# Performance work log

Measured on AMD Instinct MI355X. Metric: run time of the kernel, lower is better.

The kernel has to match this reference:

```python
import jax, jax.numpy as jnp
import numpy as np

B, H = 1_000_000, 18
TEMPERATURE = 1.0
EPS = 1e-8
NEG = -1e9  # stand-in for -inf that keeps logaddexp/exp finite


def setup_inputs() -> dict:
    key = jax.random.key(0)
    k1, k2, k3 = jax.random.split(key, 3)
    scores = jax.random.normal(k1, (B, H), dtype=jnp.float32)
    rankings = jax.random.randint(k2, (B, H), 0, 18, dtype=jnp.int32)
    mask = jax.random.randint(k3, (B, H), 0, 2, dtype=jnp.int32).astype(bool)
    return {"scores": scores, "rankings": rankings, "mask": mask}


def reference(scores, rankings, mask):
    # valid horses: masked-in and ranking >= 0
    valid = mask & (rankings >= 0)                      # (B, H) bool
    num_horses = scores.shape[1]

    # Stable sort valid horses to the front, ordered by ranking (Plackett-Luce order).
    sort_key = jnp.where(valid, rankings, num_horses + 1)
    order = jnp.argsort(sort_key, axis=1)               # stable
    s = jnp.take_along_axis(jnp.clip(scores, -10.0, 10.0), order, axis=1) / TEMPERATURE
    v = jnp.take_along_axis(valid, order, axis=1)
    s = jnp.where(v, s, NEG)                            # invalid horses contribute exp(-1e9)=0

    # Reverse cumulative logsumexp replaces the O(n^2) sequential softmax peel:
    # lse[i] = logsumexp(s[i:])  ->  log P(pick i-th) = s[i] - lse[i]
    lse = jax.lax.associative_scan(jnp.logaddexp, s, reverse=True, axis=1)
    prob = jnp.clip(jnp.exp(s - lse), EPS, 1.0 - EPS)   # matches original per-step prob clamp

    n = jnp.sum(valid, axis=1)                          # (B,) valid horse count
    # positions 0 .. n-2 contribute (last pick is deterministic)
    pos_ok = jnp.arange(num_horses)[None, :] < (n - 1)[:, None]
    race_loss = jnp.sum(jnp.where(pos_ok, -jnp.log(prob), 0.0), axis=1)

    race_valid = n >= 2                                 # races with <2 valid horses skipped
    num = jnp.sum(jnp.where(race_valid, race_loss, 0.0))
    den = jnp.sum(race_valid)
    return jnp.where(den > 0, num / jnp.maximum(den, 1).astype(num.dtype), jnp.float32(0.0))
```

## Files before the change

kernel.cpp:

```cpp
#include <hip/hip_runtime.h>
#include <stdint.h>

#define H 18
#define TPB 256
#define RPB 256

__device__ __forceinline__ void ce(unsigned long long& x, unsigned long long& y) {
    unsigned long long a = x, b = y;
    bool lt = a < b;
    x = lt ? a : b;
    y = lt ? b : a;
}

__global__ __launch_bounds__(TPB) void pl_main(const float* __restrict__ scores,
                                               const int* __restrict__ rankings,
                                               const unsigned char* __restrict__ mask8,
                                               int B,
                                               float* __restrict__ partial_loss,
                                               int* __restrict__ partial_cnt) {
    __shared__ float2 sS[RPB * 9];
    __shared__ unsigned short sK[RPB * 9];
    __shared__ int sFlag;
    __shared__ float ls[TPB / 64];
    __shared__ int   cs[TPB / 64];

    const int t = threadIdx.x;
    const int lane = t & 63;
    const int wid = t >> 6;

    if (t == 0) sFlag = 0;
    __syncthreads();
    {
        unsigned int w = reinterpret_cast<const unsigned int*>(mask8)[t];
        if (__any(w > 1u) && lane == 0) atomicOr(&sFlag, 1);
    }
    __syncthreads();
    const bool u8mode = (sFlag != 0);

    const int race0 = blockIdx.x * RPB;
    const int limit = min(RPB, B - race0);
    const int nflat2 = limit * 9;

    const float2* s2 = reinterpret_cast<const float2*>(scores) + (size_t)race0 * 9;
    const int2*   r2 = reinterpret_cast<const int2*>(rankings) + (size_t)race0 * 9;

#pragma unroll
    for (int k = 0; k < 9; ++k) {
        int f2 = k * TPB + t;
        if (f2 < nflat2) {
            sS[f2] = s2[f2];
            int2 rv = r2[f2];
            int m0, m1;
            if (u8mode) {
                uchar2 mb = *reinterpret_cast<const uchar2*>(
                    mask8 + (size_t)race0 * 18 + 2 * (size_t)f2);
                m0 = mb.x; m1 = mb.y;
            } else {
                int2 mb = reinterpret_cast<const int2*>(mask8)[(size_t)race0 * 9 + f2];
                m0 = mb.x; m1 = mb.y;
            }
            unsigned int k0 = (m0 != 0 && rv.x >= 0) ? (unsigned int)min(rv.x, 30) : 31u;
            unsigned int k1 = (m1 != 0 && rv.y >= 0) ? (unsigned int)min(rv.y, 30) : 31u;
            sK[f2] = (unsigned short)(k0 | (k1 << 8));
        }
    }
    __syncthreads();

    float th_loss = 0.0f;
    int th_cnt = 0;

    if (t < limit) {
        unsigned long long a[H];
        float m = -1e30f;
        int n = 0;
#pragma unroll
        for (int j = 0; j < 9; ++j) {
            float2 sv = sS[t * 9 + j];
            unsigned int kp = sK[t * 9 + j];
            float s0 = fminf(fmaxf(sv.x, -10.0f), 10.0f);
            float s1 = fminf(fmaxf(sv.y, -10.0f), 10.0f);
            unsigned int k0 = kp & 0xffu;
            unsigned int k1 = (kp >> 8) & 0xffu;
            if (k0 < 31u) { n++; m = fmaxf(m, s0); }
            if (k1 < 31u) { n++; m = fmaxf(m, s1); }
            unsigned int hi0 = (k0 << 5) | (unsigned int)(2 * j);
            unsigned int hi1 = (k1 << 5) | (unsigned int)(2 * j + 1);
            a[2 * j]     = ((unsigned long long)hi0 << 32) | (unsigned long long)__float_as_uint(s0);
            a[2 * j + 1] = ((unsigned long long)hi1 << 32) | (unsigned long long)__float_as_uint(s1);
        }

#pragma unroll
        for (int p = 1; p < H; p <<= 1) {
#pragma unroll
            for (int k = p; k >= 1; k >>= 1) {
#pragma unroll
                for (int j = k % p; j + k < H; j += 2 * k) {
#pragma unroll
                    for (int i = 0; i < k; ++i) {
                        if (i + j + k < H) {
                            if ((i + j) / (2 * p) == (i + j + k) / (2 * p)) {
                                ce(a[i + j], a[i + j + k]);
                            }
                        }
                    }
                }
            }
        }

        if (n >= 2) {
            float run = 0.0f;
            float loss = 0.0f;
            int cnt = 0;
#pragma unroll
            for (int q = H - 1; q >= 0; --q) {
                unsigned long long w = a[q];
                unsigned int hi = (unsigned int)(w >> 32);
                int kq = (int)(hi >> 5);
                if (kq < 31) {
                    float sv = __uint_as_float((unsigned int)w);
                    float e = __expf(sv - m);
                    run += e;
                    cnt++;
                    if (cnt > 1) {
                        float tt = m + __logf(run) - sv;
                        tt = fminf(fmaxf(tt, 1.0000000e-8f), 18.420680744f);
                        loss += tt;
                    }
                }
            }
            th_loss = loss;
            th_cnt = 1;
        }
    }

#pragma unroll
    for (int off = 32; off >= 1; off >>= 1) {
        th_loss += __shfl_down(th_loss, off);
        th_cnt  += __shfl_down(th_cnt, off);
    }
    if (lane == 0) { ls[wid] = th_loss; cs[wid] = th_cnt; }
    __syncthreads();
    if (t == 0) {
        float L = 0.0f;
        int C = 0;
#pragma unroll
        for (int w = 0; w < TPB / 64; ++w) { L += ls[w]; C += cs[w]; }
        partial_loss[blockIdx.x] = L;
        partial_cnt[blockIdx.x]  = C;
    }
}

__global__ __launch_bounds__(1024) void pl_final(const float* __restrict__ partial_loss,
                                                 const int* __restrict__ partial_cnt,
                                                 int nb, float* __restrict__ out) {
    float L = 0.0f;
    int C = 0;
    for (int i = threadIdx.x; i < nb; i += 1024) {
        L += partial_loss[i];
        C += partial_cnt[i];
    }
#pragma unroll
    for (int off = 32; off >= 1; off >>= 1) {
        L += __shfl_down(L, off);
        C += __shfl_down(C, off);
    }
    __shared__ float ls[1024 / 64];
    __shared__ int   cs[1024 / 64];
    int wid = threadIdx.x >> 6;
    int lane = threadIdx.x & 63;
    if (lane == 0) { ls[wid] = L; cs[wid] = C; }
    __syncthreads();
    if (threadIdx.x == 0) {
        float tl = 0.0f;
        int tc = 0;
#pragma unroll
        for (int w = 0; w < 1024 / 64; ++w) { tl += ls[w]; tc += cs[w]; }
        out[0] = (tc > 0) ? (tl / (float)tc) : 0.0f;
    }
}

extern "C" void kernel_launch(void* const* d_in, const int* in_sizes, int n_in,
                              void* d_out, int out_size, void* d_ws, size_t ws_size,
                              hipStream_t stream) {
    const float*         scores   = (const float*)d_in[0];
    const int*           rankings = (const int*)d_in[1];
    const unsigned char* mask     = (const unsigned char*)d_in[2];

    int B = in_sizes[0] / H;
    int nb = (B + RPB - 1) / RPB;

    float* pl = (float*)d_ws;
    int*   pc = (int*)((char*)d_ws + ((size_t)nb * sizeof(float) + 255 & ~(size_t)255));

    pl_main<<<nb, TPB, 0, stream>>>(scores, rankings, mask, B, pl, pc);
    pl_final<<<1, 1024, 0, stream>>>(pl, pc, nb, (float*)d_out);
}
```

Before: 227.7 us.

## Replace per-race sorting network with rank-bucket histogram and suffix sums

Drops the 18-element 64-bit bitonic sorting network. Each horse's exp-score is now accumulated into a per-thread shared-memory bucket indexed by its rank. A reverse prefix over the buckets gives the suffix sums used for the log-probabilities, and duplicate ranks are handled by subtracting each horse as it is consumed, in original index order, which preserves stable-sort tie-breaking. This removes the many 64-bit compare-exchanges, but adds scattered shared-memory read-modify-writes with data-dependent addresses and reuses the staging buffer behind an extra barrier.

After: 225.8 us. About the same (-0.9%).

```diff
diff --git a/kernel.cpp b/kernel.cpp
--- a/kernel.cpp
+++ b/kernel.cpp
@@ -5,21 +5,14 @@
 #define TPB 256
 #define RPB 256
 
-__device__ __forceinline__ void ce(unsigned long long& x, unsigned long long& y) {
-    unsigned long long a = x, b = y;
-    bool lt = a < b;
-    x = lt ? a : b;
-    y = lt ? b : a;
-}
-
 __global__ __launch_bounds__(TPB) void pl_main(const float* __restrict__ scores,
                                                const int* __restrict__ rankings,
                                                const unsigned char* __restrict__ mask8,
                                                int B,
                                                float* __restrict__ partial_loss,
                                                int* __restrict__ partial_cnt) {
-    __shared__ float2 sS[RPB * 9];
-    __shared__ unsigned short sK[RPB * 9];
+    __shared__ float sMem[RPB * H];
+    __shared__ unsigned short sKp[RPB * 9];
     __shared__ int sFlag;
     __shared__ float ls[TPB / 64];
     __shared__ int   cs[TPB / 64];
@@ -41,15 +34,16 @@
     const int limit = min(RPB, B - race0);
     const int nflat2 = limit * 9;
 
-    const float2* s2 = reinterpret_cast<const float2*>(scores) + (size_t)race0 * 9;
-    const int2*   r2 = reinterpret_cast<const int2*>(rankings) + (size_t)race0 * 9;
+    const float2* g_s2 = reinterpret_cast<const float2*>(scores) + (size_t)race0 * 9;
+    const int2*   g_r2 = reinterpret_cast<const int2*>(rankings) + (size_t)race0 * 9;
+    float2* sS2 = reinterpret_cast<float2*>(sMem);
 
 #pragma unroll
     for (int k = 0; k < 9; ++k) {
         int f2 = k * TPB + t;
         if (f2 < nflat2) {
-            sS[f2] = s2[f2];
-            int2 rv = r2[f2];
+            sS2[f2] = g_s2[f2];
+            int2 rv = g_r2[f2];
             int m0, m1;
             if (u8mode) {
                 uchar2 mb = *reinterpret_cast<const uchar2*>(
@@ -61,76 +55,73 @@
             }
             unsigned int k0 = (m0 != 0 && rv.x >= 0) ? (unsigned int)min(rv.x, 30) : 31u;
             unsigned int k1 = (m1 != 0 && rv.y >= 0) ? (unsigned int)min(rv.y, 30) : 31u;
-            sK[f2] = (unsigned short)(k0 | (k1 << 8));
+            sKp[f2] = (unsigned short)(k0 | (k1 << 8));
         }
     }
     __syncthreads();
 
+    float s[H];
+    int key[H];
+#pragma unroll
+    for (int j = 0; j < H; ++j) key[j] = 31;
+    float m = -1e30f;
+    int n = 0;
+    if (t < limit) {
+#pragma unroll
+        for (int j = 0; j < 9; ++j) {
+            float2 sv = sS2[t * 9 + j];
+            unsigned int kp = sKp[t * 9 + j];
+            float s0 = fminf(fmaxf(sv.x, -10.0f), 10.0f);
+            float s1 = fminf(fmaxf(sv.y, -10.0f), 10.0f);
+            int k0 = (int)(kp & 0xffu);
+            int k1 = (int)(kp >> 8);
+            s[2 * j] = s0; s[2 * j + 1] = s1;
+            key[2 * j] = k0; key[2 * j + 1] = k1;
+            if (k0 < 31) { n++; m = fmaxf(m, s0); }
+            if (k1 < 31) { n++; m = fmaxf(m, s1); }
+        }
+    }
+    __syncthreads();
+
+#pragma unroll
+    for (int r = 0; r < H; ++r) sMem[r * RPB + t] = 0.0f;
+
+#pragma unroll
+    for (int j = 0; j < H; ++j) {
+        if (key[j] < 31) {
+            int a = key[j] * RPB + t;
+            sMem[a] += __expf(s[j] - m);
+        }
+    }
+
+    {
+        float acc = 0.0f;
+#pragma unroll
+        for (int r = H - 1; r >= 0; --r) {
+            acc += sMem[r * RPB + t];
+            sMem[r * RPB + t] = acc;
+        }
+    }
+
     float th_loss = 0.0f;
     int th_cnt = 0;
-
-    if (t < limit) {
-        unsigned long long a[H];
-        float m = -1e30f;
-        int n = 0;
+    {
+        float loss = 0.0f, last_term = 0.0f;
+        int bk = -1;
 #pragma unroll
-        for (int j = 0; j < 9; ++j) {
-            float2 sv = sS[t * 9 + j];
-            unsigned int kp = sK[t * 9 + j];
-            float s0 = fminf(fmaxf(sv.x, -10.0f), 10.0f);
-            float s1 = fminf(fmaxf(sv.y, -10.0f), 10.0f);
-            unsigned int k0 = kp & 0xffu;
-            unsigned int k1 = (kp >> 8) & 0xffu;
-            if (k0 < 31u) { n++; m = fmaxf(m, s0); }
-            if (k1 < 31u) { n++; m = fmaxf(m, s1); }
-            unsigned int hi0 = (k0 << 5) | (unsigned int)(2 * j);
-            unsigned int hi1 = (k1 << 5) | (unsigned int)(2 * j + 1);
-            a[2 * j]     = ((unsigned long long)hi0 << 32) | (unsigned long long)__float_as_uint(s0);
-            a[2 * j + 1] = ((unsigned long long)hi1 << 32) | (unsigned long long)__float_as_uint(s1);
-        }
-
-#pragma unroll
-        for (int p = 1; p < H; p <<= 1) {
-#pragma unroll
-            for (int k = p; k >= 1; k >>= 1) {
-#pragma unroll
-                for (int j = k % p; j + k < H; j += 2 * k) {
-#pragma unroll
-                    for (int i = 0; i < k; ++i) {
-                        if (i + j + k < H) {
-                            if ((i + j) / (2 * p) == (i + j + k) / (2 * p)) {
-                                ce(a[i + j], a[i + j + k]);
-                            }
-                        }
-                    }
-                }
+        for (int j = 0; j < H; ++j) {
+            if (key[j] < 31) {
+                int a = key[j] * RPB + t;
+                float run = sMem[a];
+                float e = __expf(s[j] - m);
+                sMem[a] = run - e;
+                float term = m + __logf(run) - s[j];
+                term = fminf(fmaxf(term, 1.0000000e-8f), 18.420680744f);
+                loss += term;
+                if (key[j] >= bk) { bk = key[j]; last_term = term; }
             }
         }
-
-        if (n >= 2) {
-            float run = 0.0f;
-            float loss = 0.0f;
-            int cnt = 0;
-#pragma unroll
-            for (int q = H - 1; q >= 0; --q) {
-                unsigned long long w = a[q];
-                unsigned int hi = (unsigned int)(w >> 32);
-                int kq = (int)(hi >> 5);
-                if (kq < 31) {
-                    float sv = __uint_as_float((unsigned int)w);
-                    float e = __expf(sv - m);
-                    run += e;
-                    cnt++;
-                    if (cnt > 1) {
-                        float tt = m + __logf(run) - sv;
-                        tt = fminf(fmaxf(tt, 1.0000000e-8f), 18.420680744f);
-                        loss += tt;
-                    }
-                }
-            }
-            th_loss = loss;
-            th_cnt = 1;
-        }
+        if (n >= 2) { th_loss = loss - last_term; th_cnt = 1; }
     }
 
 #pragma unroll
@@ -141,8 +132,7 @@
     if (lane == 0) { ls[wid] = th_loss; cs[wid] = th_cnt; }
     __syncthreads();
     if (t == 0) {
-        float L = 0.0f;
-        int C = 0;
+        float L = 0.0f; int C = 0;
 #pragma unroll
         for (int w = 0; w < TPB / 64; ++w) { L += ls[w]; C += cs[w]; }
         partial_loss[blockIdx.x] = L;
@@ -190,7 +180,7 @@
     int nb = (B + RPB - 1) / RPB;
 
     float* pl = (float*)d_ws;
-    int*   pc = (int*)((char*)d_ws + ((size_t)nb * sizeof(float) + 255 & ~(size_t)255));
+    int*   pc = (int*)((char*)d_ws + (((size_t)nb * sizeof(float) + 255) & ~(size_t)255));
 
     pl_main<<<nb, TPB, 0, stream>>>(scores, rankings, mask, B, pl, pc);
     pl_final<<<1, 1024, 0, stream>>>(pl, pc, nb, (float*)d_out);
```
